# Kernel optimization log

Measured on AMD Instinct MI355X. Metric: run time of the kernel, lower is better.

## Reference

```python
import jax, jax.numpy as jnp
import numpy as np

B, V, L, C, H = 2, 8, 256, 1024, 16

def setup_inputs() -> dict:
    key = jax.random.key(0)
    ks = jax.random.split(key, 6)
    s = 0.02  # init scale for weights
    x = jax.random.normal(ks[0], (B, V, L, C), jnp.float32)
    Wq = jax.random.normal(ks[1], (C, C), jnp.float32) * s
    Wk = jax.random.normal(ks[2], (C, C), jnp.float32) * s
    Wv = jax.random.normal(ks[3], (C, C), jnp.float32) * s
    Wp = jax.random.normal(ks[4], (C, C), jnp.float32) * s
    bp = jnp.zeros((C,), jnp.float32)
    return {"x": x, "Wq": Wq, "Wk": Wk, "Wv": Wv, "Wp": Wp, "bp": bp}

def _view_mask(V, L):
    # view-level allow mask, expanded to token level [S, S]
    vi = jnp.arange(V)
    qv, kv = vi[:, None], vi[None, :]
    cross = ((qv == 0) & (kv == 1)) | ((qv == 1) & (kv == 0))
    later = (qv > 1) | (kv > 1)
    allow = cross | (later & (qv >= kv))  # [V, V]
    return jnp.repeat(jnp.repeat(allow, L, axis=0), L, axis=1)  # [V*L, V*L]

def reference(x, Wq, Wk, Wv, Wp, bp):
    b, v, l, c = x.shape
    h = H
    dh = c // h
    scale = dh ** -0.5
    s = v * l
    xf = x.reshape(b, s, c)
    # torch Linear: y = x @ W.T
    q = (xf @ Wq.T).reshape(b, s, h, dh).transpose(0, 2, 1, 3)  # [b,h,s,dh]
    k = (xf @ Wk.T).reshape(b, s, h, dh).transpose(0, 2, 1, 3)
    vv = (xf @ Wv.T).reshape(b, s, h, dh).transpose(0, 2, 1, 3)
    scores = jnp.einsum('bhqd,bhkd->bhqk', q, k) * scale  # [b,h,s,s]
    mask = _view_mask(v, l)
    scores = jnp.where(mask, scores, -jnp.inf)
    attn = jax.nn.softmax(scores, axis=-1)
    out = jnp.einsum('bhqk,bhkd->bhqd', attn, vv)
    out = out.transpose(0, 2, 1, 3).reshape(b, v, l, c)
    return out @ Wp.T + bp
```

## Files before the change

### kernel.cpp

```cpp
#include <hip/hip_runtime.h>
#include <stdint.h>

typedef unsigned short ushort_t;
typedef __attribute__((ext_vector_type(8))) __bf16 bf16x8;
typedef __attribute__((ext_vector_type(4))) float floatx4;
typedef __attribute__((ext_vector_type(2))) uint32_t uint32x2;

__device__ __forceinline__ ushort_t f2bf(float f) {
    uint32_t u = __builtin_bit_cast(uint32_t, f);
    u += 0x7fffu + ((u >> 16) & 1u);
    return (ushort_t)(u >> 16);
}

typedef __attribute__((address_space(1))) const void glb_void;
typedef __attribute__((address_space(3))) void lds_void;
__device__ __forceinline__ void gld16(const void* g, void* l) {
    __builtin_amdgcn_global_load_lds((glb_void*)g, (lds_void*)l, 16, 0, 0);
}

#define QSCALE 0.18033688011112042f

__global__ void cast_kernel(const float* __restrict__ x,
                            const float* __restrict__ Wq, const float* __restrict__ Wk,
                            const float* __restrict__ Wv, const float* __restrict__ Wp,
                            ushort_t* __restrict__ xb, ushort_t* __restrict__ Wqkvb,
                            ushort_t* __restrict__ Wpb)
{
    const int64_t NX = 4194304, NW = 1048576;
    int64_t i4 = ((int64_t)blockIdx.x * blockDim.x + threadIdx.x) * 4;
    const float* src; ushort_t* dst; int64_t off;
    if (i4 < NX)            { src = x;  dst = xb;          off = i4; }
    else if (i4 < NX+NW)    { src = Wq; dst = Wqkvb;       off = i4 - NX; }
    else if (i4 < NX+2*NW)  { src = Wk; dst = Wqkvb + NW;  off = i4 - NX - NW; }
    else if (i4 < NX+3*NW)  { src = Wv; dst = Wqkvb + 2*NW;off = i4 - NX - 2*NW; }
    else                    { src = Wp; dst = Wpb;         off = i4 - NX - 3*NW; }
    float4 v = *(const float4*)(src + off);
    ushort4 o;
    o.x = f2bf(v.x); o.y = f2bf(v.y); o.z = f2bf(v.z); o.w = f2bf(v.w);
    *(ushort4*)(dst + off) = o;
}

#define BM 128
#define BN 128
#define BK 32

__global__ __launch_bounds__(256, 3)
void gemm_bt(const ushort_t* __restrict__ A, const ushort_t* __restrict__ Bmat,
             int M, int N, int K, int mode,
             ushort_t* __restrict__ qb, ushort_t* __restrict__ kb, ushort_t* __restrict__ vtb,
             float* __restrict__ outf, const float* __restrict__ bias)
{
    __shared__ ushort_t As[BM * BK];
    __shared__ ushort_t Bs[BN * BK];
    const int tid  = threadIdx.x;
    const int lane = tid & 63;
    const int wave = tid >> 6;
    const int m0 = blockIdx.x * BM;
    const int n0 = blockIdx.y * BN;
    const int wrow = (wave >> 1) * 64;
    const int wcol = (wave & 1) * 64;
    const int q_ = lane >> 4;
    const int ml = lane & 15;

    floatx4 acc[4][4];
    for (int i = 0; i < 4; i++) for (int j = 0; j < 4; j++) acc[i][j] = floatx4{0.f,0.f,0.f,0.f};

    const int t0 = wave * 2, t1 = wave * 2 + 1;
    const int row_l = lane >> 2;
    const int col_l = (lane & 3) * 8;
    const ushort_t* Ag0 = A    + (int64_t)(m0 + t0*16 + row_l) * K + col_l;
    const ushort_t* Ag1 = A    + (int64_t)(m0 + t1*16 + row_l) * K + col_l;
    const ushort_t* Bg0 = Bmat + (int64_t)(n0 + t0*16 + row_l) * K + col_l;
    const ushort_t* Bg1 = Bmat + (int64_t)(n0 + t1*16 + row_l) * K + col_l;
    ushort_t* Al0 = As + t0*512; ushort_t* Al1 = As + t1*512;
    ushort_t* Bl0 = Bs + t0*512; ushort_t* Bl1 = Bs + t1*512;

    for (int k0 = 0; k0 < K; k0 += BK) {
        __syncthreads();
        gld16(Ag0 + k0, Al0);
        gld16(Ag1 + k0, Al1);
        gld16(Bg0 + k0, Bl0);
        gld16(Bg1 + k0, Bl1);
        __syncthreads();
        bf16x8 af[4], bf[4];
        for (int mt = 0; mt < 4; mt++)
            af[mt] = *(const bf16x8*)(As + (wrow + mt*16 + ml) * BK + q_*8);
        for (int nt = 0; nt < 4; nt++)
            bf[nt] = *(const bf16x8*)(Bs + (wcol + nt*16 + ml) * BK + q_*8);
        for (int mt = 0; mt < 4; mt++)
            for (int nt = 0; nt < 4; nt++)
                acc[mt][nt] = __builtin_amdgcn_mfma_f32_16x16x32_bf16(af[mt], bf[nt], acc[mt][nt], 0, 0, 0);
    }

    if (mode == 0) {
        for (int mt = 0; mt < 4; mt++) for (int nt = 0; nt < 4; nt++) {
            floatx4 v = acc[mt][nt];
            int col = n0 + wcol + nt*16 + ml;
            int which = col >> 10;
            int nn = col & 1023;
            int h = nn >> 6, d = nn & 63;
            if (which < 2) {
                ushort_t* dst = (which == 0) ? qb : kb;
                float sc = (which == 0) ? QSCALE : 1.0f;
                for (int r = 0; r < 4; r++) {
                    int rowg = m0 + wrow + mt*16 + q_*4 + r;
                    int b = rowg >> 11, s = rowg & 2047;
                    dst[(((int64_t)(b*16 + h) * 2048 + s) << 6) + d] = f2bf(v[r] * sc);
                }
            } else {
                int rowg0 = m0 + wrow + mt*16 + q_*4;
                int b = rowg0 >> 11, sbase = rowg0 & 2047;
                ushort4 o;
                o.x = f2bf(v[0]); o.y = f2bf(v[1]); o.z = f2bf(v[2]); o.w = f2bf(v[3]);
                *(ushort4*)(vtb + (((int64_t)(b*16 + h) * 64 + d) << 11) + sbase) = o;
            }
        }
    } else {
        for (int mt = 0; mt < 4; mt++) for (int nt = 0; nt < 4; nt++) {
            floatx4 v = acc[mt][nt];
            int col = n0 + wcol + nt*16 + ml;
            float bv = bias[col];
            for (int r = 0; r < 4; r++) {
                int rowg = m0 + wrow + mt*16 + q_*4 + r;
                outf[(int64_t)rowg * N + col] = v[r] + bv;
            }
        }
    }
}

__global__ __launch_bounds__(256, 3)
void attn_kernel(const ushort_t* __restrict__ Q, const ushort_t* __restrict__ Kb,
                 const ushort_t* __restrict__ Vt, ushort_t* __restrict__ Out)
{
    __shared__ ushort_t Kl[8192];
    __shared__ ushort_t Vl[8192];
    __shared__ ushort_t Pl[4 * 16 * 136];

    int bi = blockIdx.x;
    int bh = (bi & 7) + 8 * ((bi >> 3) & 3);
    int qt = (bi >> 5) & 3;
    int qv = 7 - (bi >> 7);
    int b = bh >> 4, h = bh & 15;
    int tid = threadIdx.x;
    int wave = tid >> 6, lane = tid & 63;
    int q_ = lane >> 4, ml = lane & 15;
    int rlane = lane & 15, clane = lane >> 4;
    int s0 = qv*256 + qt*64 + wave*16;

    const ushort_t* Kbh = Kb + ((int64_t)bh << 17);
    const ushort_t* Vbh = Vt + ((int64_t)bh << 17);
    ushort_t* Pw = Pl + wave * (16 * 136);

    const ushort_t* Qp = Q + (((int64_t)bh*2048 + s0 + ml) << 6) + q_*8;
    bf16x8 aq0 = *(const bf16x8*)(Qp);
    bf16x8 aq1 = *(const bf16x8*)(Qp + 32);

    floatx4 o_acc[4];
    for (int i = 0; i < 4; i++) o_acc[i] = floatx4{0.f,0.f,0.f,0.f};
    float lsum = 0.f;

    const int nviews = (qv < 2) ? 1 : (qv + 1);
    const int vfix = qv ^ 1;

    for (int vi = 0; vi < nviews; vi++) {
        int kb0 = ((nviews == 1) ? vfix : vi) * 256;
        for (int ck = 0; ck < 2; ck++) {
            int koff = kb0 + ck * 128;

            __syncthreads();
            #pragma unroll
            for (int i = 0; i < 4; i++) {
                int id = wave*4 + i;
                const ushort_t* gk = Kbh + (((int64_t)(koff + (id >> 1)*16 + rlane)) << 6)
                                         + (id & 1)*32 + clane*8;
                gld16(gk, Kl + id*512);
                const ushort_t* gv = Vbh + ((int64_t)((id & 3)*16 + rlane) << 11)
                                         + koff + (id >> 2)*32 + clane*8;
                gld16(gv, Vl + id*512);
            }
            __syncthreads();

            #pragma unroll
            for (int kt = 0; kt < 8; kt++) {
                bf16x8 k0 = *(const bf16x8*)(Kl + kt*1024 + lane*8);
                bf16x8 k1 = *(const bf16x8*)(Kl + kt*1024 + 512 + lane*8);
                floatx4 cz = floatx4{0.f,0.f,0.f,0.f};
                cz = __builtin_amdgcn_mfma_f32_16x16x32_bf16(k0, aq0, cz, 0, 0, 0);
                cz = __builtin_amdgcn_mfma_f32_16x16x32_bf16(k1, aq1, cz, 0, 0, 0);

                float p0 = __builtin_amdgcn_exp2f(cz[0]);
                float p1 = __builtin_amdgcn_exp2f(cz[1]);
                float p2 = __builtin_amdgcn_exp2f(cz[2]);
                float p3 = __builtin_amdgcn_exp2f(cz[3]);
                lsum += (p0 + p1) + (p2 + p3);
                uint32x2 wv;
                wv[0] = (uint32_t)f2bf(p0) | ((uint32_t)f2bf(p1) << 16);
                wv[1] = (uint32_t)f2bf(p2) | ((uint32_t)f2bf(p3) << 16);
                *(uint32x2*)(Pw + ml*136 + kt*16 + q_*4) = wv;
            }

            asm volatile("s_waitcnt lgkmcnt(0)" ::: "memory");

            #pragma unroll
            for (int g = 0; g < 4; g++) {
                bf16x8 ap = *(const bf16x8*)(Pw + ml*136 + g*32 + q_*8);
                #pragma unroll
                for (int dt = 0; dt < 4; dt++) {
                    bf16x8 vv = *(const bf16x8*)(Vl + (g*4 + dt)*512 + lane*8);
                    o_acc[dt] = __builtin_amdgcn_mfma_f32_16x16x32_bf16(ap, vv, o_acc[dt], 0, 0, 0);
                }
            }
        }
    }

    lsum += __shfl_xor(lsum, 16);
    lsum += __shfl_xor(lsum, 32);
    float rinv[4];
    #pragma unroll
    for (int r = 0; r < 4; r++)
        rinv[r] = 1.0f / __shfl(lsum, q_*4 + r);

    #pragma unroll
    for (int dt = 0; dt < 4; dt++)
        #pragma unroll
        for (int r = 0; r < 4; r++) {
            float v = o_acc[dt][r] * rinv[r];
            int sr = s0 + q_*4 + r;
            Out[((int64_t)b*2048 + sr) * 1024 + h*64 + dt*16 + ml] = f2bf(v);
        }
}

extern "C" void kernel_launch(void* const* d_in, const int* in_sizes, int n_in,
                              void* d_out, int out_size, void* d_ws, size_t ws_size,
                              hipStream_t stream) {
    const float* x  = (const float*)d_in[0];
    const float* Wq = (const float*)d_in[1];
    const float* Wk = (const float*)d_in[2];
    const float* Wv = (const float*)d_in[3];
    const float* Wp = (const float*)d_in[4];
    const float* bp = (const float*)d_in[5];
    float* out = (float*)d_out;

    char* ws = (char*)d_ws;
    ushort_t* xb    = (ushort_t*)(ws);
    ushort_t* Wqkvb = (ushort_t*)(ws + ((size_t)8  << 20));
    ushort_t* Wpb   = (ushort_t*)(ws + ((size_t)14 << 20));
    ushort_t* qb    = (ushort_t*)(ws + ((size_t)16 << 20));
    ushort_t* kbuf  = (ushort_t*)(ws + ((size_t)24 << 20));
    ushort_t* vtb   = (ushort_t*)(ws + ((size_t)40 << 20));
    ushort_t* attno = xb;

    cast_kernel<<<8192, 256, 0, stream>>>(x, Wq, Wk, Wv, Wp, xb, Wqkvb, Wpb);

    dim3 g0(4096 / BM, 3072 / BN);
    gemm_bt<<<g0, 256, 0, stream>>>(xb, Wqkvb, 4096, 3072, 1024, 0,
                                    qb, kbuf, vtb, nullptr, nullptr);

    attn_kernel<<<1024, 256, 0, stream>>>(qb, kbuf, vtb, attno);

    dim3 g1(4096 / BM, 1024 / BN);
    gemm_bt<<<g1, 256, 0, stream>>>(attno, Wpb, 4096, 1024, 1024, 1,
                                    nullptr, nullptr, nullptr, out, bp);
}
```

Before: 184.1 us.

## Split keys across waves in attention, prefetch K/V per wave, reduce at end

Each wave now covers all four 16-row query tiles of the block but only its own quarter of each 128-key chunk. Every wave loads and reads only its own K/V slice in LDS, so the per-chunk __syncthreads pairs are gone. The next chunk's K and V are prefetched with async LDS loads, gated by vmcnt waits, so they overlap with compute. Partial outputs and row sums are then combined across waves through LDS at the end. In exchange, accumulator registers grow fourfold (64 floats per lane), which may hurt occupancy under launch_bounds(256,3), and the final reduction adds LDS traffic.

```diff
diff --git a/kernel.cpp b/kernel.cpp
--- a/kernel.cpp
+++ b/kernel.cpp
@@ -132,102 +132,183 @@
 void attn_kernel(const ushort_t* __restrict__ Q, const ushort_t* __restrict__ Kb,
                  const ushort_t* __restrict__ Vt, ushort_t* __restrict__ Out)
 {
-    __shared__ ushort_t Kl[8192];
-    __shared__ ushort_t Vl[8192];
-    __shared__ ushort_t Pl[4 * 16 * 136];
+    __shared__ ushort_t LDS[26624];
+    ushort_t* Kl = LDS;
+    ushort_t* Vl = LDS + 8192;
 
     int bi = blockIdx.x;
     int bh = (bi & 7) + 8 * ((bi >> 3) & 3);
-    int qt = (bi >> 5) & 3;
+    int qt4 = (bi >> 5) & 3;
     int qv = 7 - (bi >> 7);
     int b = bh >> 4, h = bh & 15;
     int tid = threadIdx.x;
     int wave = tid >> 6, lane = tid & 63;
     int q_ = lane >> 4, ml = lane & 15;
     int rlane = lane & 15, clane = lane >> 4;
-    int s0 = qv*256 + qt*64 + wave*16;
+    int sB = qv*256 + qt4*64;
 
     const ushort_t* Kbh = Kb + ((int64_t)bh << 17);
     const ushort_t* Vbh = Vt + ((int64_t)bh << 17);
-    ushort_t* Pw = Pl + wave * (16 * 136);
-
-    const ushort_t* Qp = Q + (((int64_t)bh*2048 + s0 + ml) << 6) + q_*8;
-    bf16x8 aq0 = *(const bf16x8*)(Qp);
-    bf16x8 aq1 = *(const bf16x8*)(Qp + 32);
-
-    floatx4 o_acc[4];
-    for (int i = 0; i < 4; i++) o_acc[i] = floatx4{0.f,0.f,0.f,0.f};
-    float lsum = 0.f;
+    ushort_t* Pw = LDS + 16384 + wave * 2560;
+
+    bf16x8 aq0[4], aq1[4];
+    #pragma unroll
+    for (int qt = 0; qt < 4; qt++) {
+        const ushort_t* Qp = Q + (((int64_t)bh*2048 + sB + qt*16 + ml) << 6) + q_*8;
+        aq0[qt] = *(const bf16x8*)(Qp);
+        aq1[qt] = *(const bf16x8*)(Qp + 32);
+    }
+
+    floatx4 o_acc[4][4];
+    #pragma unroll
+    for (int i = 0; i < 4; i++)
+        #pragma unroll
+        for (int j = 0; j < 4; j++) o_acc[i][j] = floatx4{0.f,0.f,0.f,0.f};
+    float lsum[4] = {0.f, 0.f, 0.f, 0.f};
 
     const int nviews = (qv < 2) ? 1 : (qv + 1);
+    const int NT = nviews * 2;
     const int vfix = qv ^ 1;
 
-    for (int vi = 0; vi < nviews; vi++) {
-        int kb0 = ((nviews == 1) ? vfix : vi) * 256;
-        for (int ck = 0; ck < 2; ck++) {
-            int koff = kb0 + ck * 128;
-
-            __syncthreads();
+
+    {
+        int koff = ((nviews == 1) ? vfix : 0) * 256;
+        #pragma unroll
+        for (int i = 0; i < 4; i++) {
+            int id = wave*4 + i;
+            const ushort_t* gk = Kbh + (((int64_t)(koff + (id >> 1)*16 + rlane)) << 6)
+                                     + (id & 1)*32 + clane*8;
+            gld16(gk, Kl + id*512);
+        }
+        #pragma unroll
+        for (int i = 0; i < 4; i++) {
+            int id = wave*4 + i;
+            const ushort_t* gv = Vbh + ((int64_t)((id & 3)*16 + rlane) << 11)
+                                     + koff + (id >> 2)*32 + clane*8;
+            gld16(gv, Vl + id*512);
+        }
+    }
+
+    for (int t = 0; t < NT; ++t) {
+        asm volatile("s_waitcnt vmcnt(4)" ::: "memory");
+
+        bf16x8 kf[4];
+        kf[0] = *(const bf16x8*)(Kl + (2*wave    )*1024       + lane*8);
+        kf[1] = *(const bf16x8*)(Kl + (2*wave    )*1024 + 512 + lane*8);
+        kf[2] = *(const bf16x8*)(Kl + (2*wave + 1)*1024       + lane*8);
+        kf[3] = *(const bf16x8*)(Kl + (2*wave + 1)*1024 + 512 + lane*8);
+        asm volatile("s_waitcnt lgkmcnt(0)" ::: "memory");
+
+        if (t + 1 < NT) {
+            int koff_n = ((nviews == 1) ? vfix : ((t + 1) >> 1)) * 256 + ((t + 1) & 1) * 128;
             #pragma unroll
             for (int i = 0; i < 4; i++) {
                 int id = wave*4 + i;
-                const ushort_t* gk = Kbh + (((int64_t)(koff + (id >> 1)*16 + rlane)) << 6)
+                const ushort_t* gk = Kbh + (((int64_t)(koff_n + (id >> 1)*16 + rlane)) << 6)
                                          + (id & 1)*32 + clane*8;
                 gld16(gk, Kl + id*512);
-                const ushort_t* gv = Vbh + ((int64_t)((id & 3)*16 + rlane) << 11)
-                                         + koff + (id >> 2)*32 + clane*8;
-                gld16(gv, Vl + id*512);
-            }
-            __syncthreads();
-
-            #pragma unroll
-            for (int kt = 0; kt < 8; kt++) {
-                bf16x8 k0 = *(const bf16x8*)(Kl + kt*1024 + lane*8);
-                bf16x8 k1 = *(const bf16x8*)(Kl + kt*1024 + 512 + lane*8);
+            }
+        }
+
+        #pragma unroll
+        for (int ktl = 0; ktl < 2; ktl++) {
+            #pragma unroll
+            for (int qt = 0; qt < 4; qt++) {
                 floatx4 cz = floatx4{0.f,0.f,0.f,0.f};
-                cz = __builtin_amdgcn_mfma_f32_16x16x32_bf16(k0, aq0, cz, 0, 0, 0);
-                cz = __builtin_amdgcn_mfma_f32_16x16x32_bf16(k1, aq1, cz, 0, 0, 0);
-
+                cz = __builtin_amdgcn_mfma_f32_16x16x32_bf16(kf[ktl*2    ], aq0[qt], cz, 0, 0, 0);
+                cz = __builtin_amdgcn_mfma_f32_16x16x32_bf16(kf[ktl*2 + 1], aq1[qt], cz, 0, 0, 0);
                 float p0 = __builtin_amdgcn_exp2f(cz[0]);
                 float p1 = __builtin_amdgcn_exp2f(cz[1]);
                 float p2 = __builtin_amdgcn_exp2f(cz[2]);
                 float p3 = __builtin_amdgcn_exp2f(cz[3]);
-                lsum += (p0 + p1) + (p2 + p3);
+                lsum[qt] += (p0 + p1) + (p2 + p3);
                 uint32x2 wv;
                 wv[0] = (uint32_t)f2bf(p0) | ((uint32_t)f2bf(p1) << 16);
                 wv[1] = (uint32_t)f2bf(p2) | ((uint32_t)f2bf(p3) << 16);
-                *(uint32x2*)(Pw + ml*136 + kt*16 + q_*4) = wv;
-            }
-
-            asm volatile("s_waitcnt lgkmcnt(0)" ::: "memory");
-
-            #pragma unroll
-            for (int g = 0; g < 4; g++) {
-                bf16x8 ap = *(const bf16x8*)(Pw + ml*136 + g*32 + q_*8);
-                #pragma unroll
-                for (int dt = 0; dt < 4; dt++) {
-                    bf16x8 vv = *(const bf16x8*)(Vl + (g*4 + dt)*512 + lane*8);
-                    o_acc[dt] = __builtin_amdgcn_mfma_f32_16x16x32_bf16(ap, vv, o_acc[dt], 0, 0, 0);
-                }
-            }
-        }
-    }
-
-    lsum += __shfl_xor(lsum, 16);
-    lsum += __shfl_xor(lsum, 32);
-    float rinv[4];
-    #pragma unroll
-    for (int r = 0; r < 4; r++)
-        rinv[r] = 1.0f / __shfl(lsum, q_*4 + r);
-
-    #pragma unroll
-    for (int dt = 0; dt < 4; dt++)
-        #pragma unroll
-        for (int r = 0; r < 4; r++) {
-            float v = o_acc[dt][r] * rinv[r];
-            int sr = s0 + q_*4 + r;
-            Out[((int64_t)b*2048 + sr) * 1024 + h*64 + dt*16 + ml] = f2bf(v);
-        }
+                *(uint32x2*)(Pw + (qt*16 + ml)*40 + ktl*16 + q_*4) = wv;
+            }
+        }
+        asm volatile("s_waitcnt lgkmcnt(0)" ::: "memory");
+
+        bf16x8 ap[4];
+        #pragma unroll
+        for (int qt = 0; qt < 4; qt++)
+            ap[qt] = *(const bf16x8*)(Pw + (qt*16 + ml)*40 + q_*8);
+
+        if (t + 1 < NT) asm volatile("s_waitcnt vmcnt(4)" ::: "memory");
+        else            asm volatile("s_waitcnt vmcnt(0)" ::: "memory");
+
+        bf16x8 vv[4];
+        #pragma unroll
+        for (int dt = 0; dt < 4; dt++)
+            vv[dt] = *(const bf16x8*)(Vl + (wave*4 + dt)*512 + lane*8);
+        asm volatile("s_waitcnt lgkmcnt(0)" ::: "memory");
+
+        if (t + 1 < NT) {
+            int koff_n = ((nviews == 1) ? vfix : ((t + 1) >> 1)) * 256 + ((t + 1) & 1) * 128;
+            #pragma unroll
+            for (int i = 0; i < 4; i++) {
+                int id = wave*4 + i;
+                const ushort_t* gv = Vbh + ((int64_t)((id & 3)*16 + rlane) << 11)
+                                         + koff_n + (id >> 2)*32 + clane*8;
+                gld16(gv, Vl + id*512);
+            }
+        }
+
+        #pragma unroll
+        for (int qt = 0; qt < 4; qt++)
+            #pragma unroll
+            for (int dt = 0; dt < 4; dt++)
+                o_acc[qt][dt] = __builtin_amdgcn_mfma_f32_16x16x32_bf16(ap[qt], vv[dt], o_acc[qt][dt], 0, 0, 0);
+    }
+
+    #pragma unroll
+    for (int qt = 0; qt < 4; qt++) {
+        lsum[qt] += __shfl_xor(lsum[qt], 16);
+        lsum[qt] += __shfl_xor(lsum[qt], 32);
+    }
+
+    floatx4* red4 = (floatx4*)LDS;
+    float*   redl = (float*)LDS + 12288;
+    __syncthreads();
+    #pragma unroll
+    for (int qt = 0; qt < 4; qt++) {
+        if (qt == wave) continue;
+        int widx = wave - (wave > qt ? 1 : 0);
+        #pragma unroll
+        for (int dt = 0; dt < 4; dt++)
+            red4[(qt*3 + widx)*256 + (dt*16 + ml)*4 + q_] = o_acc[qt][dt];
+        if (q_ == 0) redl[(qt*3 + widx)*16 + ml] = lsum[qt];
+    }
+    __syncthreads();
+    #pragma unroll
+    for (int qt = 0; qt < 4; qt++) {
+        if (qt != wave) continue;
+        #pragma unroll
+        for (int j = 0; j < 3; j++) {
+            #pragma unroll
+            for (int dt = 0; dt < 4; dt++)
+                o_acc[qt][dt] += red4[(qt*3 + j)*256 + (dt*16 + ml)*4 + q_];
+            lsum[qt] += redl[(qt*3 + j)*16 + ml];
+        }
+    }
+
+    #pragma unroll
+    for (int qt = 0; qt < 4; qt++) {
+        if (qt != wave) continue;
+        float rinv[4];
+        #pragma unroll
+        for (int r = 0; r < 4; r++)
+            rinv[r] = 1.0f / __shfl(lsum[qt], q_*4 + r);
+        #pragma unroll
+        for (int dt = 0; dt < 4; dt++)
+            #pragma unroll
+            for (int r = 0; r < 4; r++) {
+                int sr = sB + qt*16 + q_*4 + r;
+                Out[((int64_t)b*2048 + sr) * 1024 + h*64 + dt*16 + ml] =
+                    f2bf(o_acc[qt][dt][r] * rinv[r]);
+            }
+    }
 }
 
 extern "C" void kernel_launch(void* const* d_in, const int* in_sizes, int n_in,
```

After: 219.0 us. 19.0% more time.
